# Optimization experiments

Hardware: AMD Instinct MI355X
Metric: run time of the kernel (lower is better)

The kernel has to match this reference:

```python
import jax, jax.numpy as jnp
import numpy as np

B, S, IN, OUT, SPLIT = 4, 2048, 4096, 4096, 1024


def setup_inputs() -> dict:
    key = jax.random.key(0)
    ks = jax.random.split(key, 14)
    def n(k, shape, scale=1.0):
        return jax.random.normal(k, shape, dtype=jnp.float32) * scale
    return {
        "x": n(ks[0], (B, S, IN)),
        "V": n(ks[1], (SPLIT, IN)),
        "U": n(ks[2], (OUT, SPLIT)),
        "v2": n(ks[3], (1, IN), 0.05),
        "v1": n(ks[4], (1, SPLIT), 0.05),
        "u2": n(ks[5], (1, SPLIT), 0.05),
        "u1": n(ks[6], (1, OUT), 0.05),
        "V_R": n(ks[7], (SPLIT, IN)),
        "U_R": n(ks[8], (OUT, SPLIT)),
        "v2_R": n(ks[9], (1, IN), 0.05),
        "v1_R": n(ks[10], (1, SPLIT), 0.05),
        "u2_R": n(ks[11], (1, SPLIT), 0.05),
        "u1_R": n(ks[12], (1, OUT), 0.05),
        "bias": n(ks[13], (OUT,), 0.02),
    }


def _quantize(w):
    # ITQ binarization: sign(w) with straight-through estimator semantics
    return w + jax.lax.stop_gradient(jnp.sign(w) - w)


def _compute_forward(x2d, V, U, v2, v1, u2, u1):
    # x2d: [T, in]; V: [split, in]; U: [out, split]
    Vq = _quantize(V)
    Uq = _quantize(U)
    v1u2 = v1 * u2  # [1, split]
    h = (x2d * v2) @ Vq.T          # [T, split]
    return (h * v1u2) @ Uq.T * u1  # [T, out]


def reference(x, V, U, v2, v1, u2, u1, V_R, U_R, v2_R, v1_R, u2_R, u1_R, bias):
    lead = x.shape[:-1]
    x2d = x.reshape(-1, x.shape[-1])
    y = _compute_forward(x2d, V, U, v2, v1, u2, u1)
    y = y + _compute_forward(x2d, V_R, U_R, v2_R, v1_R, u2_R, u1_R)
    y = y + bias
    return y.reshape(lead + (U.shape[0],))
```

## Files before the change

### kernel.cpp

```cpp
#include <hip/hip_runtime.h>


typedef __bf16 bf16x8 __attribute__((ext_vector_type(8)));
typedef float floatx4 __attribute__((ext_vector_type(4)));

__device__ __forceinline__ unsigned short f2bf_rne(float f) {
    union { float f; unsigned u; } v; v.f = f;
    unsigned r = v.u + 0x7FFFu + ((v.u >> 16) & 1u);
    return (unsigned short)(r >> 16);
}

__device__ __forceinline__ float sgnf(float w) {
    return (float)((w > 0.f) - (w < 0.f));
}

__device__ __forceinline__ void async_copy16(const void* g, void* l) {
    __builtin_amdgcn_global_load_lds(
        (const __attribute__((address_space(1))) void*)g,
        (__attribute__((address_space(3))) void*)l, 16, 0, 0);
}

#define FENCE() asm volatile("" ::: "memory")
#define BAR() do { FENCE(); __builtin_amdgcn_s_barrier(); FENCE(); } while (0)
#define VMW(N) asm volatile("s_waitcnt vmcnt(" #N ")" ::: "memory")


__global__ void cast_x_kernel(const float* __restrict__ x,
                              unsigned short* __restrict__ xb, int n4) {
    int i = blockIdx.x * blockDim.x + threadIdx.x;
    if (i >= n4) return;
    float4 v = ((const float4*)x)[i];
    ushort4 o;
    o.x = f2bf_rne(v.x); o.y = f2bf_rne(v.y);
    o.z = f2bf_rne(v.z); o.w = f2bf_rne(v.w);
    ((ushort4*)xb)[i] = o;
}

__global__ void prep_w_kernel(const float* __restrict__ V, const float* __restrict__ V_R,
                              const float* __restrict__ v2, const float* __restrict__ v2_R,
                              const float* __restrict__ U, const float* __restrict__ U_R,
                              const float* __restrict__ v1, const float* __restrict__ v1_R,
                              const float* __restrict__ u2, const float* __restrict__ u2_R,
                              const float* __restrict__ u1, const float* __restrict__ u1_R,
                              unsigned short* __restrict__ W1,
                              unsigned short* __restrict__ W2) {
    int bid = blockIdx.x;
    if (bid < 8192) {
        int i = bid * blockDim.x + threadIdx.x;
        int idx = i << 2;
        int scat = idx >> 12;
        int k = idx & 4095;
        const float* Vp; const float* sp;
        if (scat < 1024) { Vp = V + ((size_t)scat << 12); sp = v2; }
        else             { Vp = V_R + ((size_t)(scat - 1024) << 12); sp = v2_R; }
        float4 w = *(const float4*)(Vp + k);
        float4 s = *(const float4*)(sp + k);
        ushort4 o;
        o.x = f2bf_rne(sgnf(w.x) * s.x);
        o.y = f2bf_rne(sgnf(w.y) * s.y);
        o.z = f2bf_rne(sgnf(w.z) * s.z);
        o.w = f2bf_rne(sgnf(w.w) * s.w);
        ((ushort4*)W1)[i] = o;
    } else {
        int i = (bid - 8192) * blockDim.x + threadIdx.x;
        int idx = i << 2;
        int o = idx >> 11;
        int scat = idx & 2047;
        int branch = scat >> 10;
        int s = scat & 1023;
        const float* Up  = branch ? U_R  : U;
        const float* v1p = branch ? v1_R : v1;
        const float* u2p = branch ? u2_R : u2;
        float u1v = (branch ? u1_R : u1)[o];
        float4 w = *(const float4*)(Up + ((size_t)o << 10) + s);
        float4 a = *(const float4*)(v1p + s);
        float4 b = *(const float4*)(u2p + s);
        ushort4 out;
        out.x = f2bf_rne(sgnf(w.x) * a.x * b.x * u1v);
        out.y = f2bf_rne(sgnf(w.y) * a.y * b.y * u1v);
        out.z = f2bf_rne(sgnf(w.z) * a.z * b.z * u1v);
        out.w = f2bf_rne(sgnf(w.w) * a.w * b.w * u1v);
        ((ushort4*)W2)[i] = out;
    }
}


template <bool OUT_BF16, bool ADD_BIAS>
__global__ __launch_bounds__(512, 2)
void gemm256(const unsigned short* __restrict__ A,
             const unsigned short* __restrict__ B,
             void* __restrict__ Cv,
             const float* __restrict__ bias,
             int M, int N, int K, int ntn) {
    (void)M;
    __shared__ __align__(16) unsigned short As[2][256 * 64];
    __shared__ __align__(16) unsigned short Bs[2][256 * 64];

    const int tid = threadIdx.x;
    const int lane = tid & 63;
    const int wave = tid >> 6;
    const int warp_m = wave >> 2;
    const int warp_n = wave & 3;

    const int nwg = gridDim.x;
    const int hw = blockIdx.x;
    const int swz = (hw & 7) * (nwg >> 3) + (hw >> 3);
    const int tm = swz / ntn;
    const int tn = swz - tm * ntn;
    const int m0 = tm << 8;
    const int n0 = tn << 8;

    const int srow = tid >> 3;
    const int scg8 = (((tid & 7) ^ (srow & 7)) << 3);
    const size_t aTB = (size_t)(m0 + srow) * (size_t)K + scg8;
    const size_t bTB = (size_t)(n0 + srow) * (size_t)K + scg8;
    const int ldst = tid << 3;

    auto stageA = [&](int buf, int blk, int kt) {
        async_copy16(A + aTB + ((size_t)(blk << 6)) * (size_t)K + (kt << 6),
                     &As[buf][(blk << 12) + ldst]);
    };
    auto stageB = [&](int buf, int blk, int kt) {
        async_copy16(B + bTB + ((size_t)(blk << 6)) * (size_t)K + (kt << 6),
                     &Bs[buf][(blk << 12) + ldst]);
    };

    const int fm = lane & 15;
    const int cgl = lane >> 4;
    const int key = fm & 7;
    const int ok0 = ((cgl ^ key) << 3);
    const int ok1 = (((4 | cgl) ^ key) << 3);
    const int arow0 = (warp_m << 7) + fm;
    const int brow0 = (warp_n << 6) + fm;

    auto lda = [&](bf16x8 (&dst)[4][2], int c, int mh) {
#pragma unroll
        for (int mi = 0; mi < 4; ++mi) {
            const unsigned short* p = &As[c][(arow0 + (mh << 6) + (mi << 4)) << 6];
            dst[mi][0] = *(const bf16x8*)(p + ok0);
            dst[mi][1] = *(const bf16x8*)(p + ok1);
        }
    };
    auto ldb = [&](bf16x8 (&dst)[2][2], int c, int nh) {
#pragma unroll
        for (int ni = 0; ni < 2; ++ni) {
            const unsigned short* p = &Bs[c][(brow0 + (nh << 5) + (ni << 4)) << 6];
            dst[ni][0] = *(const bf16x8*)(p + ok0);
            dst[ni][1] = *(const bf16x8*)(p + ok1);
        }
    };

    floatx4 acc[8][4];
#pragma unroll
    for (int i = 0; i < 8; ++i)
#pragma unroll
        for (int j = 0; j < 4; ++j)
#pragma unroll
            for (int r = 0; r < 4; ++r) acc[i][j][r] = 0.f;

    bf16x8 a0[4][2], a1[4][2], b0[2][2], b1[2][2];

#define MMAQ(aS, bS, MH, NH) do { \
    __builtin_amdgcn_s_setprio(1); \
    _Pragma("unroll") \
    for (int mi_ = 0; mi_ < 4; ++mi_) { \
      _Pragma("unroll") \
      for (int ni_ = 0; ni_ < 2; ++ni_) { \
        acc[(MH)*4 + mi_][(NH)*2 + ni_] = __builtin_amdgcn_mfma_f32_16x16x32_bf16( \
            aS[mi_][0], bS[ni_][0], acc[(MH)*4 + mi_][(NH)*2 + ni_], 0, 0, 0); \
        acc[(MH)*4 + mi_][(NH)*2 + ni_] = __builtin_amdgcn_mfma_f32_16x16x32_bf16( \
            aS[mi_][1], bS[ni_][1], acc[(MH)*4 + mi_][(NH)*2 + ni_], 0, 0, 0); \
      } } \
    __builtin_amdgcn_s_setprio(0); \
  } while (0)

#pragma unroll
    for (int blk = 0; blk < 4; ++blk) stageA(0, blk, 0);
#pragma unroll
    for (int blk = 0; blk < 4; ++blk) stageB(0, blk, 0);
    VMW(0);
    BAR();
    lda(a0, 0, 0);
    ldb(b0, 0, 0);

    const int NT = K >> 6;
    for (int t = 0; t < NT - 1; ++t) {
        const int c = t & 1, nc = c ^ 1;
        stageA(nc, 0, t + 1); stageA(nc, 2, t + 1);
        stageB(nc, 0, t + 1); stageB(nc, 1, t + 1);
        stageB(nc, 2, t + 1); stageB(nc, 3, t + 1);
        ldb(b1, c, 1);
        MMAQ(a0, b0, 0, 0);
        VMW(6);
        BAR();
        lda(a1, c, 1);
        MMAQ(a0, b1, 0, 1);
        VMW(0);
        BAR();
        MMAQ(a1, b1, 1, 1);
        stageA(nc, 1, t + 1); stageA(nc, 3, t + 1);
        bf16x8 a0n[4][2], b0n[2][2];
        lda(a0n, nc, 0);
        ldb(b0n, nc, 0);
        MMAQ(a1, b0, 1, 0);
        BAR();
#pragma unroll
        for (int mi = 0; mi < 4; ++mi) { a0[mi][0] = a0n[mi][0]; a0[mi][1] = a0n[mi][1]; }
#pragma unroll
        for (int ni = 0; ni < 2; ++ni) { b0[ni][0] = b0n[ni][0]; b0[ni][1] = b0n[ni][1]; }
    }
    {
        const int c = (NT - 1) & 1;
        ldb(b1, c, 1);
        MMAQ(a0, b0, 0, 0);
        VMW(0);
        BAR();
        lda(a1, c, 1);
        MMAQ(a0, b1, 0, 1);
        MMAQ(a1, b1, 1, 1);
        MMAQ(a1, b0, 1, 0);
    }
#undef MMAQ

    const int rq = (lane >> 4) << 2;
    const int col = lane & 15;
#pragma unroll
    for (int mi = 0; mi < 8; ++mi) {
#pragma unroll
        for (int r = 0; r < 4; ++r) {
            const int gm = m0 + (warp_m << 7) + (mi << 4) + rq + r;
            const size_t base = (size_t)gm * (size_t)N;
#pragma unroll
            for (int ni = 0; ni < 4; ++ni) {
                const int gn = n0 + (warp_n << 6) + (ni << 4) + col;
                float v = acc[mi][ni][r];
                if (ADD_BIAS) v += bias[gn];
                if (OUT_BF16)
                    ((unsigned short*)Cv)[base + gn] = f2bf_rne(v);
                else
                    ((float*)Cv)[base + gn] = v;
            }
        }
    }
}


extern "C" void kernel_launch(void* const* d_in, const int* in_sizes, int n_in,
                              void* d_out, int out_size, void* d_ws, size_t ws_size,
                              hipStream_t stream) {
    const float* x    = (const float*)d_in[0];
    const float* V    = (const float*)d_in[1];
    const float* U    = (const float*)d_in[2];
    const float* v2   = (const float*)d_in[3];
    const float* v1   = (const float*)d_in[4];
    const float* u2   = (const float*)d_in[5];
    const float* u1   = (const float*)d_in[6];
    const float* V_R  = (const float*)d_in[7];
    const float* U_R  = (const float*)d_in[8];
    const float* v2_R = (const float*)d_in[9];
    const float* v1_R = (const float*)d_in[10];
    const float* u2_R = (const float*)d_in[11];
    const float* u1_R = (const float*)d_in[12];
    const float* bias = (const float*)d_in[13];
    float* out = (float*)d_out;

    char* ws = (char*)d_ws;
    unsigned short* Xb = (unsigned short*)ws;
    unsigned short* W1 = (unsigned short*)(ws + (size_t)67108864);
    unsigned short* W2 = (unsigned short*)(ws + (size_t)67108864 + 16777216);
    unsigned short* H  = (unsigned short*)(ws + (size_t)67108864 + 33554432);

    cast_x_kernel<<<32768, 256, 0, stream>>>(x, Xb, 8388608);
    prep_w_kernel<<<16384, 256, 0, stream>>>(V, V_R, v2, v2_R,
                                             U, U_R, v1, v1_R, u2, u2_R, u1, u1_R,
                                             W1, W2);

    gemm256<true, false><<<dim3(256), 512, 0, stream>>>(Xb, W1, (void*)H, nullptr,
                                                        8192, 2048, 4096, 8);
    gemm256<false, true><<<dim3(512), 512, 0, stream>>>(H, W2, (void*)out, bias,
                                                        8192, 4096, 2048, 16);
}
```

Baseline: 618.0 us.

## Restructure GEMM main loop into HipKittens-style 8-wave ping-pong schedule

Splits the LDS tiles into per-half sub-buffers and rewrites the K loop to process two K-tiles per iteration. Global-to-LDS loads for tile t+2 are interleaved between MFMA quadrants, with explicit barriers and lgkmcnt waits around each quadrant. The aim is to overlap memory traffic with MFMA work more evenly and to drop the register copies of the prefetched fragments. In exchange it adds many more barriers per iteration, which could serialize the waves, and it assumes an even NT.

```diff
diff --git a/kernel.cpp b/kernel.cpp
--- a/kernel.cpp
+++ b/kernel.cpp
@@ -23,6 +23,7 @@
 #define FENCE() asm volatile("" ::: "memory")
 #define BAR() do { FENCE(); __builtin_amdgcn_s_barrier(); FENCE(); } while (0)
 #define VMW(N) asm volatile("s_waitcnt vmcnt(" #N ")" ::: "memory")
+#define LGKM(N) asm volatile("s_waitcnt lgkmcnt(" #N ")" ::: "memory")
 
 
 __global__ void cast_x_kernel(const float* __restrict__ x,
@@ -93,8 +94,8 @@
              const float* __restrict__ bias,
              int M, int N, int K, int ntn) {
     (void)M;
-    __shared__ __align__(16) unsigned short As[2][256 * 64];
-    __shared__ __align__(16) unsigned short Bs[2][256 * 64];
+    __shared__ __align__(16) unsigned short As[2][2][128 * 64];
+    __shared__ __align__(16) unsigned short Bs[2][2][128 * 64];
 
     const int tid = threadIdx.x;
     const int lane = tid & 63;
@@ -112,17 +113,18 @@
 
     const int srow = tid >> 3;
     const int scg8 = (((tid & 7) ^ (srow & 7)) << 3);
-    const size_t aTB = (size_t)(m0 + srow) * (size_t)K + scg8;
-    const size_t bTB = (size_t)(n0 + srow) * (size_t)K + scg8;
     const int ldst = tid << 3;
-
-    auto stageA = [&](int buf, int blk, int kt) {
-        async_copy16(A + aTB + ((size_t)(blk << 6)) * (size_t)K + (kt << 6),
-                     &As[buf][(blk << 12) + ldst]);
+    const size_t Ks = (size_t)K;
+
+    auto stA = [&](int buf, int h, int kt) {
+        const unsigned short* g = A + (size_t)(m0 + (h << 7) + srow) * Ks + (kt << 6) + scg8;
+        async_copy16(g,             &As[buf][h][ldst]);
+        async_copy16(g + (Ks << 6), &As[buf][h][4096 + ldst]);
     };
-    auto stageB = [&](int buf, int blk, int kt) {
-        async_copy16(B + bTB + ((size_t)(blk << 6)) * (size_t)K + (kt << 6),
-                     &Bs[buf][(blk << 12) + ldst]);
+    auto stB = [&](int buf, int h, int kt) {
+        const unsigned short* g = B + (size_t)(n0 + (h << 7) + srow) * Ks + (kt << 6) + scg8;
+        async_copy16(g,             &Bs[buf][h][ldst]);
+        async_copy16(g + (Ks << 6), &Bs[buf][h][4096 + ldst]);
     };
 
     const int fm = lane & 15;
@@ -130,21 +132,21 @@
     const int key = fm & 7;
     const int ok0 = ((cgl ^ key) << 3);
     const int ok1 = (((4 | cgl) ^ key) << 3);
-    const int arow0 = (warp_m << 7) + fm;
-    const int brow0 = (warp_n << 6) + fm;
-
-    auto lda = [&](bf16x8 (&dst)[4][2], int c, int mh) {
+
+    auto lda = [&](bf16x8 (&dst)[4][2], int buf, int mh) {
+        const unsigned short* base = &As[buf][warp_m][0];
 #pragma unroll
         for (int mi = 0; mi < 4; ++mi) {
-            const unsigned short* p = &As[c][(arow0 + (mh << 6) + (mi << 4)) << 6];
+            const unsigned short* p = base + (((mh << 6) + (mi << 4) + fm) << 6);
             dst[mi][0] = *(const bf16x8*)(p + ok0);
             dst[mi][1] = *(const bf16x8*)(p + ok1);
         }
     };
-    auto ldb = [&](bf16x8 (&dst)[2][2], int c, int nh) {
+    auto ldb = [&](bf16x8 (&dst)[2][2], int buf, int nh) {
+        const unsigned short* base = &Bs[buf][warp_n >> 1][0];
 #pragma unroll
         for (int ni = 0; ni < 2; ++ni) {
-            const unsigned short* p = &Bs[c][(brow0 + (nh << 5) + (ni << 4)) << 6];
+            const unsigned short* p = base + ((((warp_n & 1) << 6) + (nh << 5) + (ni << 4) + fm) << 6);
             dst[ni][0] = *(const bf16x8*)(p + ok0);
             dst[ni][1] = *(const bf16x8*)(p + ok1);
         }
@@ -174,48 +176,71 @@
     __builtin_amdgcn_s_setprio(0); \
   } while (0)
 
-#pragma unroll
-    for (int blk = 0; blk < 4; ++blk) stageA(0, blk, 0);
-#pragma unroll
-    for (int blk = 0; blk < 4; ++blk) stageB(0, blk, 0);
-    VMW(0);
+    stB(0, 0, 0); stB(0, 1, 0); stA(0, 0, 0); stA(0, 1, 0);
+    stB(1, 0, 1); stB(1, 1, 1); stA(1, 0, 1); stA(1, 1, 1);
+    VMW(8);
     BAR();
-    lda(a0, 0, 0);
-    ldb(b0, 0, 0);
 
     const int NT = K >> 6;
-    for (int t = 0; t < NT - 1; ++t) {
-        const int c = t & 1, nc = c ^ 1;
-        stageA(nc, 0, t + 1); stageA(nc, 2, t + 1);
-        stageB(nc, 0, t + 1); stageB(nc, 1, t + 1);
-        stageB(nc, 2, t + 1); stageB(nc, 3, t + 1);
-        ldb(b1, c, 1);
+    for (int i = 0; i < (NT >> 1) - 1; ++i) {
+        const int t2k = 2 * i + 2, t3k = 2 * i + 3;
+        lda(a0, 0, 0); ldb(b0, 0, 0);
+        BAR(); LGKM(0);
         MMAQ(a0, b0, 0, 0);
-        VMW(6);
-        BAR();
-        lda(a1, c, 1);
+        BAR();
+        ldb(b1, 0, 1);
+        BAR(); LGKM(0);
         MMAQ(a0, b1, 0, 1);
-        VMW(0);
-        BAR();
+        BAR();
+        lda(a1, 0, 1);
+        stB(0, 0, t2k); stB(0, 1, t2k);
+        BAR(); LGKM(0);
         MMAQ(a1, b1, 1, 1);
-        stageA(nc, 1, t + 1); stageA(nc, 3, t + 1);
-        bf16x8 a0n[4][2], b0n[2][2];
-        lda(a0n, nc, 0);
-        ldb(b0n, nc, 0);
+        BAR();
+        stA(0, 0, t2k); stA(0, 1, t2k);
+        VMW(8);
+        BAR();
         MMAQ(a1, b0, 1, 0);
         BAR();
-#pragma unroll
-        for (int mi = 0; mi < 4; ++mi) { a0[mi][0] = a0n[mi][0]; a0[mi][1] = a0n[mi][1]; }
-#pragma unroll
-        for (int ni = 0; ni < 2; ++ni) { b0[ni][0] = b0n[ni][0]; b0[ni][1] = b0n[ni][1]; }
+        lda(a0, 1, 0); ldb(b0, 1, 0);
+        BAR(); LGKM(0);
+        MMAQ(a0, b0, 0, 0);
+        BAR();
+        ldb(b1, 1, 1);
+        BAR(); LGKM(0);
+        MMAQ(a0, b1, 0, 1);
+        BAR();
+        lda(a1, 1, 1);
+        stB(1, 0, t3k); stB(1, 1, t3k);
+        BAR(); LGKM(0);
+        MMAQ(a1, b1, 1, 1);
+        BAR();
+        stA(1, 0, t3k); stA(1, 1, t3k);
+        VMW(8);
+        BAR();
+        MMAQ(a1, b0, 1, 0);
+        BAR();
     }
     {
-        const int c = (NT - 1) & 1;
-        ldb(b1, c, 1);
+        lda(a0, 0, 0); ldb(b0, 0, 0);
+        BAR(); LGKM(0);
         MMAQ(a0, b0, 0, 0);
+        BAR();
+        ldb(b1, 0, 1);
+        BAR(); LGKM(0);
+        MMAQ(a0, b1, 0, 1);
+        BAR();
+        lda(a1, 0, 1);
+        BAR(); LGKM(0);
+        MMAQ(a1, b1, 1, 1);
+        BAR();
         VMW(0);
         BAR();
-        lda(a1, c, 1);
+        MMAQ(a1, b0, 1, 0);
+        BAR();
+        lda(a0, 1, 0); ldb(b0, 1, 0);
+        ldb(b1, 1, 1); lda(a1, 1, 1);
+        MMAQ(a0, b0, 0, 0);
         MMAQ(a0, b1, 0, 1);
         MMAQ(a1, b1, 1, 1);
         MMAQ(a1, b0, 1, 0);
```

Result: faster. 536.8 us (-13.1%).
